# Kernel tuning notes

Hardware: AMD Instinct MI355X
Metric: run time of the kernel (lower is better)

Reference implementation:

```python
import jax, jax.numpy as jnp
import numpy as np


def setup_inputs() -> dict:
    key = jax.random.key(0)
    k = jax.random.split(key, 6)
    B, N, Cin, Cd, nE = 64, 197, 768, 256, 8192
    return {
        "z": jax.random.normal(k[0], (B, N, Cin), dtype=jnp.float32),
        "emb": jax.random.truncated_normal(k[1], -3.0, 3.0, (nE, Cd), dtype=jnp.float32),
        "W_compress": jax.random.normal(k[2], (Cin, Cd), dtype=jnp.float32) * 0.02,
        "b_compress": jnp.zeros((Cd,), dtype=jnp.float32),
        "W_expand": jax.random.normal(k[3], (Cd, Cin), dtype=jnp.float32) * 0.02,
        "b_expand": jnp.zeros((Cin,), dtype=jnp.float32),
    }


def reference(z, emb, W_compress, b_compress, W_expand, b_expand):
    # compress: [B,N,Cin] -> [B,N,Cd]
    zc = jnp.einsum('bnc,cd->bnd', z, W_compress) + b_compress
    zf = zc.reshape(-1, zc.shape[-1])  # [M, Cd]
    # squared distances to codebook: ||z||^2 + ||e||^2 - 2 z.e  -> [M, nE]
    d = (jnp.sum(zf * zf, axis=1, keepdims=True)
         + jnp.sum(emb * emb, axis=1)
         - 2.0 * (zf @ emb.T))
    indices = jnp.argmin(d, axis=1)  # [M]
    z_q = emb[indices]               # gather [M, Cd]
    sg = jax.lax.stop_gradient
    # training-mode commitment/codebook loss
    loss = jnp.mean((sg(z_q) - zf) ** 2) + 2.0 * jnp.mean((z_q - sg(zf)) ** 2)
    # straight-through estimator
    z_q = sg(z_q) + zf - sg(zf)
    z_q = z_q.reshape(zc.shape)
    out = jnp.einsum('bnd,dc->bnc', z_q, W_expand) + b_expand  # [B,N,Cin]
    return (out, loss)
```

## Files before the change

### kernel.cpp

```cpp
#include <hip/hip_runtime.h>
#include <stdint.h>

#define M_TOK 12608
#define MPAD  12672
#define CIN   768
#define CD    256
#define NE    8192
#define NCHUNK 8
#define CHUNK  1024

typedef unsigned long long u64;
typedef unsigned int u32;
typedef _Float16 f16;
typedef _Float16 f16x8 __attribute__((ext_vector_type(8)));
typedef _Float16 f16x4 __attribute__((ext_vector_type(4)));
typedef float f32x4 __attribute__((ext_vector_type(4)));

#if __has_builtin(__builtin_amdgcn_global_load_lds)
#define HAVE_GLL 1
#else
#define HAVE_GLL 0
#endif

__device__ __forceinline__ void stage16(const f16* src, char* lds_base, int lane)
{
#if HAVE_GLL
    __builtin_amdgcn_global_load_lds(
        (__attribute__((address_space(1))) void*)(src),
        (__attribute__((address_space(3))) void*)(lds_base), 16, 0, 0);
#else
    *(f16x8*)(lds_base + lane * 16) = *(const f16x8*)src;
#endif
}

__global__ __launch_bounds__(256) void k_prep(const float* __restrict__ emb,
                                              const float* __restrict__ Wc,
                                              const float* __restrict__ We,
                                              const float* __restrict__ z,
                                              float* __restrict__ enorm,
                                              f16* __restrict__ embf16,
                                              f16* __restrict__ wchi,
                                              f16* __restrict__ wclo,
                                              f16* __restrict__ wet,
                                              f16* __restrict__ zhi,
                                              f16* __restrict__ zlo,
                                              float* __restrict__ loss_slot)
{
    const int b = blockIdx.x;
    const int t = threadIdx.x;
    if (b < 2048) {
        if (b == 0 && t == 0) *loss_slot = 0.0f;
        int row  = b * 4 + (t >> 6);
        int lane = t & 63;
        float4 v = *(const float4*)&emb[(size_t)row * CD + lane * 4];
        f16x4 hv = { (f16)v.x, (f16)v.y, (f16)v.z, (f16)v.w };
        *(f16x4*)&embf16[(size_t)row * CD + lane * 4] = hv;
        float s = v.x*v.x + v.y*v.y + v.z*v.z + v.w*v.w;
        #pragma unroll
        for (int o = 32; o; o >>= 1) s += __shfl_down(s, o, 64);
        if (lane == 0) enorm[row] = s;
    } else if (b < 2048 + 768) {
        int tid = (b - 2048) * 256 + t;
        {
            int n = tid & 255, k = tid >> 8;
            float v = Wc[(size_t)k * CD + n];
            f16 h = (f16)v;
            wchi[(size_t)n * CIN + k] = h;
            wclo[(size_t)n * CIN + k] = (f16)(v - (float)h);
        }
        {
            int d = tid / CIN, c = tid - d * CIN;
            wet[(size_t)c * CD + d] = (f16)We[(size_t)d * CIN + c];
        }
    } else {
        size_t i4 = (size_t)(b - 2816) * 256 + t;
        float4 v = ((const float4*)z)[i4];
        f16x4 h = { (f16)v.x, (f16)v.y, (f16)v.z, (f16)v.w };
        f16x4 lo = { (f16)(v.x - (float)h.x), (f16)(v.y - (float)h.y),
                     (f16)(v.z - (float)h.z), (f16)(v.w - (float)h.w) };
        ((f16x4*)zhi)[i4] = h;
        ((f16x4*)zlo)[i4] = lo;
    }
}

__global__ __launch_bounds__(256) void k_compress_f(const f16* __restrict__ zhi,
                                                    const f16* __restrict__ zlo,
                                                    const f16* __restrict__ wchi,
                                                    const f16* __restrict__ wclo,
                                                    const float* __restrict__ bc,
                                                    float* __restrict__ zc,
                                                    f16* __restrict__ zcf16)
{
    __shared__ __align__(16) f16 Ah[128 * 64];
    __shared__ __align__(16) f16 Al[128 * 64];
    __shared__ __align__(16) f16 Bh[64 * 64];
    __shared__ __align__(16) f16 Bl[64 * 64];

    const int t = threadIdx.x;
    const int w = t >> 6, l = t & 63;
    const int wrow = w * 32;
    const int m0   = blockIdx.x * 128;
    const int col0 = blockIdx.y * 64;

    const int cg   = (t & 7) ^ ((t >> 3) & 7);
    const int rloc = t >> 3;
    const f16* ahsrc[4]; const f16* alsrc[4];
    #pragma unroll
    for (int i = 0; i < 4; ++i) {
        int am = m0 + i * 32 + rloc; am = am < M_TOK ? am : (M_TOK - 1);
        ahsrc[i] = zhi + (size_t)am * CIN + cg * 8;
        alsrc[i] = zlo + (size_t)am * CIN + cg * 8;
    }
    const f16* bhsrc[2]; const f16* blsrc[2];
    #pragma unroll
    for (int i = 0; i < 2; ++i) {
        int br = col0 + i * 32 + rloc;
        bhsrc[i] = wchi + (size_t)br * CIN + cg * 8;
        blsrc[i] = wclo + (size_t)br * CIN + cg * 8;
    }

    f32x4 acc[2][4];
    #pragma unroll
    for (int a = 0; a < 2; ++a)
        #pragma unroll
        for (int b2 = 0; b2 < 4; ++b2) acc[a][b2] = (f32x4){0.f,0.f,0.f,0.f};

    for (int ks = 0; ks < CIN / 64; ++ks) {
        __syncthreads();
        #pragma unroll
        for (int i = 0; i < 4; ++i) {
            stage16(ahsrc[i] + ks * 64, (char*)Ah + (i * 256 + w * 64) * 16, l);
            stage16(alsrc[i] + ks * 64, (char*)Al + (i * 256 + w * 64) * 16, l);
        }
        #pragma unroll
        for (int i = 0; i < 2; ++i) {
            stage16(bhsrc[i] + ks * 64, (char*)Bh + (i * 256 + w * 64) * 16, l);
            stage16(blsrc[i] + ks * 64, (char*)Bl + (i * 256 + w * 64) * 16, l);
        }
        __syncthreads();
        #pragma unroll
        for (int kk = 0; kk < 2; ++kk) {
            const int pofs = ((kk * 4 + (l >> 4)) ^ (l & 7)) * 16;
            f16x8 ah[2], al[2], bh[4], bl[4];
            #pragma unroll
            for (int tm = 0; tm < 2; ++tm) {
                ah[tm] = *(const f16x8*)((const char*)Ah + (wrow + tm*16 + (l & 15)) * 128 + pofs);
                al[tm] = *(const f16x8*)((const char*)Al + (wrow + tm*16 + (l & 15)) * 128 + pofs);
            }
            #pragma unroll
            for (int tn = 0; tn < 4; ++tn) {
                bh[tn] = *(const f16x8*)((const char*)Bh + (tn*16 + (l & 15)) * 128 + pofs);
                bl[tn] = *(const f16x8*)((const char*)Bl + (tn*16 + (l & 15)) * 128 + pofs);
            }
            #pragma unroll
            for (int tm = 0; tm < 2; ++tm)
                #pragma unroll
                for (int tn = 0; tn < 4; ++tn) {
                    f32x4 a = acc[tm][tn];
                    a = __builtin_amdgcn_mfma_f32_16x16x32_f16(ah[tm], bh[tn], a, 0, 0, 0);
                    a = __builtin_amdgcn_mfma_f32_16x16x32_f16(ah[tm], bl[tn], a, 0, 0, 0);
                    a = __builtin_amdgcn_mfma_f32_16x16x32_f16(al[tm], bh[tn], a, 0, 0, 0);
                    acc[tm][tn] = a;
                }
        }
    }

    #pragma unroll
    for (int tm = 0; tm < 2; ++tm) {
        #pragma unroll
        for (int reg = 0; reg < 4; ++reg) {
            int row = m0 + wrow + tm * 16 + (l >> 4) * 4 + reg;
            if (row < M_TOK) {
                #pragma unroll
                for (int tn = 0; tn < 4; ++tn) {
                    int col = col0 + tn * 16 + (l & 15);
                    float v = acc[tm][tn][reg] + bc[col];
                    zc[(size_t)row * CD + col] = v;
                    zcf16[(size_t)row * CD + col] = (f16)v;
                }
            }
        }
    }
}

__global__ __launch_bounds__(256, 2) void k_dist_mfma(const f16* __restrict__ zcf16,
                                                      const f16* __restrict__ embf16,
                                                      const float* __restrict__ enorm,
                                                      u64* __restrict__ part)
{
    __shared__ __align__(16) f16 Bs[64 * 256];
    __shared__ u64 wred[128][2][2];

    const int t = threadIdx.x;
    const int w = t >> 6, l = t & 63;
    const int rg  = w >> 1;
    const int cgp = w & 1;
    const int m0    = blockIdx.x * 128;
    const int chunk = blockIdx.y;
    const int jbase = chunk * CHUNK;

    f16x8 afr[4][8];
    #pragma unroll
    for (int h = 0; h < 2; ++h) {
        __syncthreads();
        #pragma unroll
        for (int i = 0; i < 8; ++i) {
            int r = (w * 8 + i) * 2 + (l >> 5);
            int c = (l & 31) ^ (r & 7);
            int gr = m0 + h * 64 + r; gr = gr < M_TOK ? gr : (M_TOK - 1);
            stage16(zcf16 + (size_t)gr * CD + c * 8, (char*)Bs + (w * 8 + i) * 1024, l);
        }
        __syncthreads();
        if (rg == h) {
            #pragma unroll
            for (int mb = 0; mb < 4; ++mb) {
                int rl = mb * 16 + (l & 15);
                #pragma unroll
                for (int ks = 0; ks < 8; ++ks) {
                    int pc = (ks * 4 + (l >> 4)) ^ (rl & 7);
                    afr[mb][ks] = *(const f16x8*)((const char*)Bs + rl * 512 + pc * 16);
                }
            }
        }
    }

    float bd[2][16];
    #pragma unroll
    for (int sc = 0; sc < 2; ++sc)
        #pragma unroll
        for (int s = 0; s < 16; ++s) bd[sc][s] = __builtin_inff();

    for (int jt = 0; jt < 16; ++jt) {
        const int j0 = jbase + jt * 64;
        __syncthreads();
        #pragma unroll
        for (int i = 0; i < 8; ++i) {
            int r = (w * 8 + i) * 2 + (l >> 5);
            int c = (l & 31) ^ (r & 7);
            stage16(embf16 + (size_t)(j0 + r) * CD + c * 8,
                    (char*)Bs + (w * 8 + i) * 1024, l);
        }
        __syncthreads();

        #pragma unroll
        for (int sc = 0; sc < 2; ++sc) {
            const int colrow = cgp * 32 + sc * 16 + (l & 15);
            f32x4 acc[4];
            #pragma unroll
            for (int mb = 0; mb < 4; ++mb) acc[mb] = (f32x4){0.f,0.f,0.f,0.f};
            #pragma unroll
            for (int ks = 0; ks < 8; ++ks) {
                int pc = (ks * 4 + (l >> 4)) ^ (colrow & 7);
                f16x8 bf = *(const f16x8*)((const char*)Bs + colrow * 512 + pc * 16);
                #pragma unroll
                for (int mb = 0; mb < 4; ++mb)
                    acc[mb] = __builtin_amdgcn_mfma_f32_16x16x32_f16(afr[mb][ks], bf, acc[mb], 0, 0, 0);
            }
            float en = enorm[j0 + colrow];
            #pragma unroll
            for (int mb = 0; mb < 4; ++mb) {
                #pragma unroll
                for (int reg = 0; reg < 4; ++reg) {
                    float d = fmaf(acc[mb][reg], -2.f, en);
                    float ds = __uint_as_float((__float_as_uint(d) & ~15u) | (u32)jt);
                    float cur = bd[sc][mb * 4 + reg];
                    bd[sc][mb * 4 + reg] = ds < cur ? ds : cur;
                }
            }
        }
    }

    #pragma unroll
    for (int mb = 0; mb < 4; ++mb) {
        #pragma unroll
        for (int reg = 0; reg < 4; ++reg) {
            u64 key[2];
            #pragma unroll
            for (int sc = 0; sc < 2; ++sc) {
                u32 bits = __float_as_uint(bd[sc][mb * 4 + reg]);
                int jtb  = (int)(bits & 15u);
                int col  = jbase + jtb * 64 + cgp * 32 + sc * 16 + (l & 15);
                u32 u = (bits & 0x80000000u) ? ~bits : (bits | 0x80000000u);
                key[sc] = ((u64)u << 32) | (u32)col;
            }
            u64 b  = key[0] < key[1] ? key[0] : key[1];
            u64 s2 = key[0] < key[1] ? key[1] : key[0];
            #pragma unroll
            for (int off = 1; off <= 8; off <<= 1) {
                u64 ob = __shfl_xor(b, off, 64);
                u64 os = __shfl_xor(s2, off, 64);
                u64 nb = b < ob ? b : ob;
                u64 mx = b < ob ? ob : b;
                s2 = s2 < os ? s2 : os;
                s2 = s2 < mx ? s2 : mx;
                b = nb;
            }
            if ((l & 15) == 0) {
                int row = rg * 64 + mb * 16 + (l >> 4) * 4 + reg;
                wred[row][cgp][0] = b;
                wred[row][cgp][1] = s2;
            }
        }
    }
    __syncthreads();
    if (t < 128) {
        u64 b0 = wred[t][0][0], s0 = wred[t][0][1];
        u64 b1 = wred[t][1][0], s1 = wred[t][1][1];
        u64 B  = b0 < b1 ? b0 : b1;
        u64 mx = b0 < b1 ? b1 : b0;
        u64 S  = s0 < s1 ? s0 : s1;
        S = S < mx ? S : mx;
        int row = m0 + t;
        if (row < M_TOK) {
            part[((size_t)row * NCHUNK + chunk) * 2 + 0] = B;
            part[((size_t)row * NCHUNK + chunk) * 2 + 1] = S;
        }
    }
}

__global__ __launch_bounds__(256) void k_rescore(const float* __restrict__ zc,
                                                 const float* __restrict__ emb,
                                                 const float* __restrict__ enorm,
                                                 const u64* __restrict__ part,
                                                 int* __restrict__ idxp,
                                                 float* __restrict__ loss_slot)
{
    const int row = blockIdx.x * 4 + (threadIdx.x >> 6);
    const int l   = threadIdx.x & 63;
    const int c   = l & 15;
    const int q   = l >> 4;
    __shared__ float lsum[4];

    u64 key = part[(size_t)row * 16 + c];
    int col = (int)((u32)key & (NE - 1));
    const float4* ep = (const float4*)emb + (size_t)col * 64 + q * 16;
    const float4* zp = (const float4*)zc  + (size_t)row * 64 + q * 16;

    float p = 0.f, zn = 0.f;
    #pragma unroll
    for (int i = 0; i < 16; ++i) {
        float4 e = ep[i], zv = zp[i];
        p  = fmaf(e.x, zv.x, fmaf(e.y, zv.y, fmaf(e.z, zv.z, fmaf(e.w, zv.w, p))));
        zn = fmaf(zv.x, zv.x, fmaf(zv.y, zv.y, fmaf(zv.z, zv.z, fmaf(zv.w, zv.w, zn))));
    }
    p  += __shfl_xor(p, 16, 64);  p  += __shfl_xor(p, 32, 64);
    zn += __shfl_xor(zn, 16, 64); zn += __shfl_xor(zn, 32, 64);

    float d = fmaf(p, -2.f, enorm[col]);
    u32 u = __float_as_uint(d);
    u = (u & 0x80000000u) ? ~u : (u | 0x80000000u);
    u64 best = ((u64)u << 32) | (u32)col;
    #pragma unroll
    for (int off = 1; off <= 8; off <<= 1) {
        u64 ob = __shfl_xor(best, off, 64);
        best = ob < best ? ob : best;
    }

    u32 hi = (u32)(best >> 32);
    float dbest = (hi & 0x80000000u) ? __uint_as_float(hi & 0x7fffffffu)
                                     : __uint_as_float(~hi);
    if (l == 0) {
        idxp[row] = (int)((u32)best & (NE - 1));
        lsum[threadIdx.x >> 6] = dbest + zn;
    }
    __syncthreads();
    if (threadIdx.x == 0) {
        float tot = lsum[0] + lsum[1] + lsum[2] + lsum[3];
        atomicAdd(loss_slot, tot * (3.0f / 3227648.0f));
    }
}

__global__ __launch_bounds__(256) void k_expand_mfma(const f16* __restrict__ embf16,
                                                     const int* __restrict__ idxp,
                                                     const f16* __restrict__ wet,
                                                     const float* __restrict__ be,
                                                     float* __restrict__ out)
{
    __shared__ __align__(16) f16 As[128 * 64];
    __shared__ __align__(16) f16 Bs[128 * 64];

    const int t = threadIdx.x;
    const int w = t >> 6, l = t & 63;
    const int wrow = (w >> 1) * 64, wcol = (w & 1) * 64;
    const int m0   = blockIdx.x * 128;
    const int col0 = blockIdx.y * 128;

    const int cg   = (t & 7) ^ ((t >> 3) & 7);
    const int rloc = t >> 3;
    const f16* asrc[4]; const f16* bsrc[4];
    #pragma unroll
    for (int i = 0; i < 4; ++i) {
        int r = i * 32 + rloc;
        int m = m0 + r; m = m < M_TOK ? m : (M_TOK - 1);
        int er = idxp[m];
        asrc[i] = embf16 + (size_t)er * CD + cg * 8;
        bsrc[i] = wet + (size_t)(col0 + r) * CD + cg * 8;
    }
    const int prd0 = (l >> 4) ^ (l & 7);
    const int prd1 = (4 + (l >> 4)) ^ (l & 7);

    f32x4 acc[4][4];
    #pragma unroll
    for (int a = 0; a < 4; ++a)
        #pragma unroll
        for (int b = 0; b < 4; ++b) acc[a][b] = (f32x4){0.f,0.f,0.f,0.f};

    for (int ks = 0; ks < 4; ++ks) {
        __syncthreads();
        #pragma unroll
        for (int i = 0; i < 4; ++i) {
            stage16(asrc[i] + ks * 64, (char*)As + (i * 256 + w * 64) * 16, l);
            stage16(bsrc[i] + ks * 64, (char*)Bs + (i * 256 + w * 64) * 16, l);
        }
        __syncthreads();
        #pragma unroll
        for (int kk = 0; kk < 2; ++kk) {
            const int pofs = (kk ? prd1 : prd0) * 16;
            f16x8 af[4], bf[4];
            #pragma unroll
            for (int tm = 0; tm < 4; ++tm)
                af[tm] = *(const f16x8*)((const char*)As + (wrow + tm*16 + (l & 15)) * 128 + pofs);
            #pragma unroll
            for (int tn = 0; tn < 4; ++tn)
                bf[tn] = *(const f16x8*)((const char*)Bs + (wcol + tn*16 + (l & 15)) * 128 + pofs);
            #pragma unroll
            for (int tm = 0; tm < 4; ++tm)
                #pragma unroll
                for (int tn = 0; tn < 4; ++tn)
                    acc[tm][tn] = __builtin_amdgcn_mfma_f32_16x16x32_f16(af[tm], bf[tn], acc[tm][tn], 0, 0, 0);
        }
    }

    float bev[4];
    #pragma unroll
    for (int tn = 0; tn < 4; ++tn) bev[tn] = be[col0 + wcol + tn * 16 + (l & 15)];
    #pragma unroll
    for (int tm = 0; tm < 4; ++tm) {
        #pragma unroll
        for (int reg = 0; reg < 4; ++reg) {
            int row = m0 + wrow + tm * 16 + (l >> 4) * 4 + reg;
            if (row < M_TOK) {
                #pragma unroll
                for (int tn = 0; tn < 4; ++tn) {
                    int col = col0 + wcol + tn * 16 + (l & 15);
                    out[(size_t)row * CIN + col] = acc[tm][tn][reg] + bev[tn];
                }
            }
        }
    }
}

#define BK1 16
__global__ __launch_bounds__(256) void k_compress(const float* __restrict__ z,
                                                  const float* __restrict__ W,
                                                  const float* __restrict__ bias,
                                                  float* __restrict__ zc,
                                                  f16* __restrict__ zcf16)
{
    __shared__ __align__(16) float As[BK1][64 + 4];
    __shared__ __align__(16) float Bs[BK1][64 + 4];
    const int t  = threadIdx.x;
    const int tx = t & 15, ty = t >> 4;
    const int row0 = blockIdx.x * 64;
    const int col0 = blockIdx.y * 64;

    const int la_r = t >> 2;
    const int la_k = (t & 3) << 2;
    const int lb_k = t >> 4;
    const int lb_n = (t & 15) << 2;

    float acc[4][4] = {};

    for (int k0 = 0; k0 < CIN; k0 += BK1) {
        float4 a4 = *(const float4*)&z[(size_t)(row0 + la_r) * CIN + k0 + la_k];
        float4 b4 = *(const float4*)&W[(size_t)(k0 + lb_k) * CD + col0 + lb_n];
        __syncthreads();
        As[la_k + 0][la_r] = a4.x; As[la_k + 1][la_r] = a4.y;
        As[la_k + 2][la_r] = a4.z; As[la_k + 3][la_r] = a4.w;
        *(float4*)&Bs[lb_k][lb_n] = b4;
        __syncthreads();
        #pragma unroll
        for (int k = 0; k < BK1; ++k) {
            float a[4], b[4];
            *(float4*)&a[0] = *(const float4*)&As[k][ty * 4];
            *(float4*)&b[0] = *(const float4*)&Bs[k][tx * 4];
            #pragma unroll
            for (int i = 0; i < 4; ++i)
                #pragma unroll
                for (int j = 0; j < 4; ++j)
                    acc[i][j] = fmaf(a[i], b[j], acc[i][j]);
        }
    }

    float4 bb = *(const float4*)&bias[col0 + tx * 4];
    #pragma unroll
    for (int i = 0; i < 4; ++i) {
        float4 v;
        v.x = acc[i][0] + bb.x; v.y = acc[i][1] + bb.y;
        v.z = acc[i][2] + bb.z; v.w = acc[i][3] + bb.w;
        size_t off = (size_t)(row0 + ty * 4 + i) * CD + col0 + tx * 4;
        *(float4*)&zc[off] = v;
        f16x4 hv = { (f16)v.x, (f16)v.y, (f16)v.z, (f16)v.w };
        *(f16x4*)&zcf16[off] = hv;
    }
}

extern "C" void kernel_launch(void* const* d_in, const int* in_sizes, int n_in,
                              void* d_out, int out_size, void* d_ws, size_t ws_size,
                              hipStream_t stream)
{
    (void)in_sizes; (void)n_in; (void)out_size;

    const float* z   = (const float*)d_in[0];
    const float* emb = (const float*)d_in[1];
    const float* Wc  = (const float*)d_in[2];
    const float* bc  = (const float*)d_in[3];
    const float* We  = (const float*)d_in[4];
    const float* be  = (const float*)d_in[5];

    float* out       = (float*)d_out;
    float* loss_slot = out + (size_t)M_TOK * CIN;

    char* base = (char*)d_ws;
    size_t off = 0;
    auto align_up = [](size_t x) { return (x + 255) & ~(size_t)255; };

    float* enorm = (float*)(base + off); off = align_up(off + (size_t)NE * 4);
    u64*   part  = (u64*)(base + off);   off = align_up(off + (size_t)M_TOK * 16 * 8);
    int*   idxp  = (int*)(base + off);   off = align_up(off + (size_t)M_TOK * 4);
    f16*   embf16= (f16*)(base + off);   off = align_up(off + (size_t)NE * CD * 2);
    f16*   zcf16 = (f16*)(base + off);   off = align_up(off + (size_t)MPAD * CD * 2);
    f16*   wet   = (f16*)(base + off);   off = align_up(off + (size_t)CIN * CD * 2);
    f16*   wchi  = (f16*)(base + off);   off = align_up(off + (size_t)CD * CIN * 2);
    f16*   wclo  = (f16*)(base + off);   off = align_up(off + (size_t)CD * CIN * 2);

    const size_t zsplit_bytes = (size_t)M_TOK * CIN * 2;
    bool have_split = (ws_size >= off + 2 * zsplit_bytes);
    f16 *zhi = nullptr, *zlo = nullptr;
    if (have_split) {
        zhi = (f16*)(base + off); off = align_up(off + zsplit_bytes);
        zlo = (f16*)(base + off); off = align_up(off + zsplit_bytes);
    }
    const size_t zc_bytes = (size_t)M_TOK * CD * 4;
    float* zc = (ws_size >= off + zc_bytes) ? (float*)(base + off) : out;

    if (have_split) {
        k_prep      <<<12272, 256, 0, stream>>>(emb, Wc, We, z, enorm, embf16,
                                                wchi, wclo, wet, zhi, zlo, loss_slot);
        k_compress_f<<<dim3(MPAD / 128, CD / 64), 256, 0, stream>>>(zhi, zlo, wchi, wclo,
                                                                    bc, zc, zcf16);
    } else {
        k_prep    <<<2816, 256, 0, stream>>>(emb, Wc, We, z, enorm, embf16,
                                             wchi, wclo, wet, (f16*)wchi, (f16*)wclo, loss_slot);
        k_compress<<<dim3(M_TOK / 64, CD / 64), 256, 0, stream>>>(z, Wc, bc, zc, zcf16);
    }

    k_dist_mfma  <<<dim3(MPAD / 128, NCHUNK), 256, 0, stream>>>(zcf16, embf16, enorm, part);
    k_rescore    <<<M_TOK / 4, 256, 0, stream>>>(zc, emb, enorm, part, idxp, loss_slot);
    k_expand_mfma<<<dim3(MPAD / 128, CIN / 128), 256, 0, stream>>>(embf16, idxp, wet, be, out);
}
```

Measured before the change: 277.2 us.

## Stream codebook fragments from global into registers, dropping LDS staging in dist and expand

The distance kernel now keeps a 64-row A tile in registers and gives each wave its own 256-column slice of the codebook chunk. B fragments are loaded straight from global memory into registers, with the next tile prefetched, so the per-tile LDS staging and barriers disappear. The expand kernel is rebuilt the same way: a 64-row gathered A tile and per-wave 192-column slices of the weight, one block per row tile. The cost is that B is read from global/L2 without LDS sharing, and the grid has twice the blocks for distance and fewer, longer blocks for expand.

```diff
diff --git a/kernel.cpp b/kernel.cpp
--- a/kernel.cpp
+++ b/kernel.cpp
@@ -188,103 +188,84 @@
                                                       const float* __restrict__ enorm,
                                                       u64* __restrict__ part)
 {
-    __shared__ __align__(16) f16 Bs[64 * 256];
-    __shared__ u64 wred[128][2][2];
+    __shared__ __align__(16) f16 Abuf[64 * 256];
+    __shared__ u64 wred[64][4][2];
 
     const int t = threadIdx.x;
     const int w = t >> 6, l = t & 63;
-    const int rg  = w >> 1;
-    const int cgp = w & 1;
-    const int m0    = blockIdx.x * 128;
+    const int m0    = blockIdx.x * 64;
     const int chunk = blockIdx.y;
-    const int jbase = chunk * CHUNK;
-
+    const int jb    = chunk * CHUNK + w * 256;
+
+    #pragma unroll
+    for (int i = 0; i < 8; ++i) {
+        int r = (w * 8 + i) * 2 + (l >> 5);
+        int c = (l & 31) ^ (r & 7);
+        int gr = m0 + r; gr = gr < M_TOK ? gr : (M_TOK - 1);
+        stage16(zcf16 + (size_t)gr * CD + c * 8, (char*)Abuf + (w * 8 + i) * 1024, l);
+    }
+    __syncthreads();
     f16x8 afr[4][8];
     #pragma unroll
-    for (int h = 0; h < 2; ++h) {
-        __syncthreads();
-        #pragma unroll
-        for (int i = 0; i < 8; ++i) {
-            int r = (w * 8 + i) * 2 + (l >> 5);
-            int c = (l & 31) ^ (r & 7);
-            int gr = m0 + h * 64 + r; gr = gr < M_TOK ? gr : (M_TOK - 1);
-            stage16(zcf16 + (size_t)gr * CD + c * 8, (char*)Bs + (w * 8 + i) * 1024, l);
-        }
-        __syncthreads();
-        if (rg == h) {
-            #pragma unroll
-            for (int mb = 0; mb < 4; ++mb) {
-                int rl = mb * 16 + (l & 15);
-                #pragma unroll
-                for (int ks = 0; ks < 8; ++ks) {
-                    int pc = (ks * 4 + (l >> 4)) ^ (rl & 7);
-                    afr[mb][ks] = *(const f16x8*)((const char*)Bs + rl * 512 + pc * 16);
-                }
-            }
-        }
-    }
-
-    float bd[2][16];
-    #pragma unroll
-    for (int sc = 0; sc < 2; ++sc)
-        #pragma unroll
-        for (int s = 0; s < 16; ++s) bd[sc][s] = __builtin_inff();
+    for (int mb = 0; mb < 4; ++mb) {
+        int rl = mb * 16 + (l & 15);
+        #pragma unroll
+        for (int ks = 0; ks < 8; ++ks) {
+            int pc = (ks * 4 + (l >> 4)) ^ (rl & 7);
+            afr[mb][ks] = *(const f16x8*)((const char*)Abuf + rl * 512 + pc * 16);
+        }
+    }
+    asm volatile("" ::: "memory");
+
+    float bd[16];
+    #pragma unroll
+    for (int s = 0; s < 16; ++s) bd[s] = __builtin_inff();
+
+    const f16* bpbase = embf16 + (size_t)(jb + (l & 15)) * CD + (l >> 4) * 8;
+    f16x8 bf[8];
+    #pragma unroll
+    for (int ks = 0; ks < 8; ++ks) bf[ks] = *(const f16x8*)(bpbase + ks * 32);
 
     for (int jt = 0; jt < 16; ++jt) {
-        const int j0 = jbase + jt * 64;
-        __syncthreads();
-        #pragma unroll
-        for (int i = 0; i < 8; ++i) {
-            int r = (w * 8 + i) * 2 + (l >> 5);
-            int c = (l & 31) ^ (r & 7);
-            stage16(embf16 + (size_t)(j0 + r) * CD + c * 8,
-                    (char*)Bs + (w * 8 + i) * 1024, l);
-        }
-        __syncthreads();
-
-        #pragma unroll
-        for (int sc = 0; sc < 2; ++sc) {
-            const int colrow = cgp * 32 + sc * 16 + (l & 15);
-            f32x4 acc[4];
-            #pragma unroll
-            for (int mb = 0; mb < 4; ++mb) acc[mb] = (f32x4){0.f,0.f,0.f,0.f};
-            #pragma unroll
-            for (int ks = 0; ks < 8; ++ks) {
-                int pc = (ks * 4 + (l >> 4)) ^ (colrow & 7);
-                f16x8 bf = *(const f16x8*)((const char*)Bs + colrow * 512 + pc * 16);
-                #pragma unroll
-                for (int mb = 0; mb < 4; ++mb)
-                    acc[mb] = __builtin_amdgcn_mfma_f32_16x16x32_f16(afr[mb][ks], bf, acc[mb], 0, 0, 0);
-            }
-            float en = enorm[j0 + colrow];
-            #pragma unroll
-            for (int mb = 0; mb < 4; ++mb) {
-                #pragma unroll
-                for (int reg = 0; reg < 4; ++reg) {
-                    float d = fmaf(acc[mb][reg], -2.f, en);
-                    float ds = __uint_as_float((__float_as_uint(d) & ~15u) | (u32)jt);
-                    float cur = bd[sc][mb * 4 + reg];
-                    bd[sc][mb * 4 + reg] = ds < cur ? ds : cur;
-                }
-            }
-        }
+        f16x8 bfn[8];
+        const f16* bpn = bpbase + (size_t)(((jt + 1) & 15) * 16) * CD;
+        #pragma unroll
+        for (int ks = 0; ks < 8; ++ks) bfn[ks] = *(const f16x8*)(bpn + ks * 32);
+
+        f32x4 acc[4];
+        #pragma unroll
+        for (int mb = 0; mb < 4; ++mb) acc[mb] = (f32x4){0.f,0.f,0.f,0.f};
+        #pragma unroll
+        for (int ks = 0; ks < 8; ++ks)
+            #pragma unroll
+            for (int mb = 0; mb < 4; ++mb)
+                acc[mb] = __builtin_amdgcn_mfma_f32_16x16x32_f16(afr[mb][ks], bf[ks], acc[mb], 0, 0, 0);
+
+        float en = enorm[jb + jt * 16 + (l & 15)];
+        #pragma unroll
+        for (int mb = 0; mb < 4; ++mb) {
+            #pragma unroll
+            for (int reg = 0; reg < 4; ++reg) {
+                float d = fmaf(acc[mb][reg], -2.f, en);
+                float ds = __uint_as_float((__float_as_uint(d) & ~15u) | (u32)jt);
+                float cur = bd[mb * 4 + reg];
+                bd[mb * 4 + reg] = ds < cur ? ds : cur;
+            }
+        }
+        #pragma unroll
+        for (int ks = 0; ks < 8; ++ks) bf[ks] = bfn[ks];
     }
 
     #pragma unroll
     for (int mb = 0; mb < 4; ++mb) {
         #pragma unroll
         for (int reg = 0; reg < 4; ++reg) {
-            u64 key[2];
-            #pragma unroll
-            for (int sc = 0; sc < 2; ++sc) {
-                u32 bits = __float_as_uint(bd[sc][mb * 4 + reg]);
-                int jtb  = (int)(bits & 15u);
-                int col  = jbase + jtb * 64 + cgp * 32 + sc * 16 + (l & 15);
-                u32 u = (bits & 0x80000000u) ? ~bits : (bits | 0x80000000u);
-                key[sc] = ((u64)u << 32) | (u32)col;
-            }
-            u64 b  = key[0] < key[1] ? key[0] : key[1];
-            u64 s2 = key[0] < key[1] ? key[1] : key[0];
+            u32 bits = __float_as_uint(bd[mb * 4 + reg]);
+            int jtb  = (int)(bits & 15u);
+            int col  = jb + jtb * 16 + (l & 15);
+            u32 u = (bits & 0x80000000u) ? ~bits : (bits | 0x80000000u);
+            u64 b  = ((u64)u << 32) | (u32)col;
+            u64 s2 = ~0ull;
             #pragma unroll
             for (int off = 1; off <= 8; off <<= 1) {
                 u64 ob = __shfl_xor(b, off, 64);
@@ -296,24 +277,25 @@
                 b = nb;
             }
             if ((l & 15) == 0) {
-                int row = rg * 64 + mb * 16 + (l >> 4) * 4 + reg;
-                wred[row][cgp][0] = b;
-                wred[row][cgp][1] = s2;
+                int row = mb * 16 + (l >> 4) * 4 + reg;
+                wred[row][w][0] = b;
+                wred[row][w][1] = s2;
             }
         }
     }
     __syncthreads();
-    if (t < 128) {
-        u64 b0 = wred[t][0][0], s0 = wred[t][0][1];
-        u64 b1 = wred[t][1][0], s1 = wred[t][1][1];
-        u64 B  = b0 < b1 ? b0 : b1;
-        u64 mx = b0 < b1 ? b1 : b0;
-        u64 S  = s0 < s1 ? s0 : s1;
-        S = S < mx ? S : mx;
+    if (t < 64) {
+        u64 best = wred[t][0][0], sec = wred[t][0][1];
+        #pragma unroll
+        for (int c = 1; c < 4; ++c) {
+            u64 b = wred[t][c][0], s = wred[t][c][1];
+            if (b < best) { sec = (best < s) ? best : s; best = b; }
+            else if (b < sec) { sec = b; }
+        }
         int row = m0 + t;
         if (row < M_TOK) {
-            part[((size_t)row * NCHUNK + chunk) * 2 + 0] = B;
-            part[((size_t)row * NCHUNK + chunk) * 2 + 1] = S;
+            part[((size_t)row * NCHUNK + chunk) * 2 + 0] = best;
+            part[((size_t)row * NCHUNK + chunk) * 2 + 1] = sec;
         }
     }
 }
@@ -370,83 +352,73 @@
     }
 }
 
-__global__ __launch_bounds__(256) void k_expand_mfma(const f16* __restrict__ embf16,
-                                                     const int* __restrict__ idxp,
-                                                     const f16* __restrict__ wet,
-                                                     const float* __restrict__ be,
-                                                     float* __restrict__ out)
-{
-    __shared__ __align__(16) f16 As[128 * 64];
-    __shared__ __align__(16) f16 Bs[128 * 64];
+__global__ __launch_bounds__(256, 2) void k_expand_mfma(const f16* __restrict__ embf16,
+                                                        const int* __restrict__ idxp,
+                                                        const f16* __restrict__ wet,
+                                                        const float* __restrict__ be,
+                                                        float* __restrict__ out)
+{
+    __shared__ __align__(16) f16 Abuf[64 * 256];
 
     const int t = threadIdx.x;
     const int w = t >> 6, l = t & 63;
-    const int wrow = (w >> 1) * 64, wcol = (w & 1) * 64;
-    const int m0   = blockIdx.x * 128;
-    const int col0 = blockIdx.y * 128;
-
-    const int cg   = (t & 7) ^ ((t >> 3) & 7);
-    const int rloc = t >> 3;
-    const f16* asrc[4]; const f16* bsrc[4];
-    #pragma unroll
-    for (int i = 0; i < 4; ++i) {
-        int r = i * 32 + rloc;
+    const int m0 = blockIdx.x * 64;
+
+    #pragma unroll
+    for (int i = 0; i < 8; ++i) {
+        int r = (w * 8 + i) * 2 + (l >> 5);
         int m = m0 + r; m = m < M_TOK ? m : (M_TOK - 1);
         int er = idxp[m];
-        asrc[i] = embf16 + (size_t)er * CD + cg * 8;
-        bsrc[i] = wet + (size_t)(col0 + r) * CD + cg * 8;
-    }
-    const int prd0 = (l >> 4) ^ (l & 7);
-    const int prd1 = (4 + (l >> 4)) ^ (l & 7);
-
-    f32x4 acc[4][4];
-    #pragma unroll
-    for (int a = 0; a < 4; ++a)
-        #pragma unroll
-        for (int b = 0; b < 4; ++b) acc[a][b] = (f32x4){0.f,0.f,0.f,0.f};
-
-    for (int ks = 0; ks < 4; ++ks) {
-        __syncthreads();
-        #pragma unroll
-        for (int i = 0; i < 4; ++i) {
-            stage16(asrc[i] + ks * 64, (char*)As + (i * 256 + w * 64) * 16, l);
-            stage16(bsrc[i] + ks * 64, (char*)Bs + (i * 256 + w * 64) * 16, l);
-        }
-        __syncthreads();
-        #pragma unroll
-        for (int kk = 0; kk < 2; ++kk) {
-            const int pofs = (kk ? prd1 : prd0) * 16;
-            f16x8 af[4], bf[4];
-            #pragma unroll
-            for (int tm = 0; tm < 4; ++tm)
-                af[tm] = *(const f16x8*)((const char*)As + (wrow + tm*16 + (l & 15)) * 128 + pofs);
-            #pragma unroll
-            for (int tn = 0; tn < 4; ++tn)
-                bf[tn] = *(const f16x8*)((const char*)Bs + (wcol + tn*16 + (l & 15)) * 128 + pofs);
-            #pragma unroll
-            for (int tm = 0; tm < 4; ++tm)
-                #pragma unroll
-                for (int tn = 0; tn < 4; ++tn)
-                    acc[tm][tn] = __builtin_amdgcn_mfma_f32_16x16x32_f16(af[tm], bf[tn], acc[tm][tn], 0, 0, 0);
-        }
-    }
-
-    float bev[4];
-    #pragma unroll
-    for (int tn = 0; tn < 4; ++tn) bev[tn] = be[col0 + wcol + tn * 16 + (l & 15)];
-    #pragma unroll
-    for (int tm = 0; tm < 4; ++tm) {
-        #pragma unroll
-        for (int reg = 0; reg < 4; ++reg) {
-            int row = m0 + wrow + tm * 16 + (l >> 4) * 4 + reg;
-            if (row < M_TOK) {
-                #pragma unroll
-                for (int tn = 0; tn < 4; ++tn) {
-                    int col = col0 + wcol + tn * 16 + (l & 15);
-                    out[(size_t)row * CIN + col] = acc[tm][tn][reg] + bev[tn];
-                }
-            }
-        }
+        int c = (l & 31) ^ (r & 7);
+        stage16(embf16 + (size_t)er * CD + c * 8, (char*)Abuf + (w * 8 + i) * 1024, l);
+    }
+    __syncthreads();
+    f16x8 afr[4][8];
+    #pragma unroll
+    for (int mb = 0; mb < 4; ++mb) {
+        int rl = mb * 16 + (l & 15);
+        #pragma unroll
+        for (int ks = 0; ks < 8; ++ks) {
+            int pc = (ks * 4 + (l >> 4)) ^ (rl & 7);
+            afr[mb][ks] = *(const f16x8*)((const char*)Abuf + rl * 512 + pc * 16);
+        }
+    }
+    asm volatile("" ::: "memory");
+
+    const int colw = w * 192;
+    const f16* bpbase = wet + (size_t)(colw + (l & 15)) * CD + (l >> 4) * 8;
+    f16x8 bf[8];
+    #pragma unroll
+    for (int ks = 0; ks < 8; ++ks) bf[ks] = *(const f16x8*)(bpbase + ks * 32);
+
+    for (int jt = 0; jt < 12; ++jt) {
+        f16x8 bfn[8];
+        const f16* bpn = bpbase + (size_t)((jt + 1 < 12 ? jt + 1 : 0) * 16) * CD;
+        #pragma unroll
+        for (int ks = 0; ks < 8; ++ks) bfn[ks] = *(const f16x8*)(bpn + ks * 32);
+
+        f32x4 acc[4];
+        #pragma unroll
+        for (int mb = 0; mb < 4; ++mb) acc[mb] = (f32x4){0.f,0.f,0.f,0.f};
+        #pragma unroll
+        for (int ks = 0; ks < 8; ++ks)
+            #pragma unroll
+            for (int mb = 0; mb < 4; ++mb)
+                acc[mb] = __builtin_amdgcn_mfma_f32_16x16x32_f16(afr[mb][ks], bf[ks], acc[mb], 0, 0, 0);
+
+        int col = colw + jt * 16 + (l & 15);
+        float bev = be[col];
+        #pragma unroll
+        for (int mb = 0; mb < 4; ++mb) {
+            #pragma unroll
+            for (int reg = 0; reg < 4; ++reg) {
+                int row = m0 + mb * 16 + (l >> 4) * 4 + reg;
+                if (row < M_TOK)
+                    out[(size_t)row * CIN + col] = acc[mb][reg] + bev;
+            }
+        }
+        #pragma unroll
+        for (int ks = 0; ks < 8; ++ks) bf[ks] = bfn[ks];
     }
 }
 
@@ -555,7 +527,7 @@
         k_compress<<<dim3(M_TOK / 64, CD / 64), 256, 0, stream>>>(z, Wc, bc, zc, zcf16);
     }
 
-    k_dist_mfma  <<<dim3(MPAD / 128, NCHUNK), 256, 0, stream>>>(zcf16, embf16, enorm, part);
+    k_dist_mfma  <<<dim3(MPAD / 64, NCHUNK), 256, 0, stream>>>(zcf16, embf16, enorm, part);
     k_rescore    <<<M_TOK / 4, 256, 0, stream>>>(zc, emb, enorm, part, idxp, loss_slot);
-    k_expand_mfma<<<dim3(MPAD / 128, CIN / 128), 256, 0, stream>>>(embf16, idxp, wet, be, out);
-}
+    k_expand_mfma<<<MPAD / 64, 256, 0, stream>>>(embf16, idxp, wet, be, out);
+}
```

New measurement: 348.3 us. 25.7% more time.
